# Kernel tuning notes

Measured on AMD Instinct MI355X. Metric: run time of the kernel, lower is better.

## Reference

```python
import jax, jax.numpy as jnp
from jax import lax
import numpy as np

WS = 32          # window size
NUM_AA = 21      # one-hot alphabet size (hardcoded in original forward)
L = 2048         # sequence length
WIDTH = 2048
IN_SIZE = WS * NUM_AA + WS  # 704


def setup_inputs() -> dict:
    key = jax.random.key(0)
    ks = jax.random.split(key, 8)
    x = jax.random.randint(ks[0], (L,), 0, NUM_AA, dtype=jnp.int32)
    gain = np.sqrt(2.0)  # relu gain, xavier_normal init
    def xavier(k, fan_out, fan_in):
        std = gain * np.sqrt(2.0 / (fan_in + fan_out))
        return jax.random.normal(k, (fan_out, fan_in), dtype=jnp.float32) * std
    inp = {"x": x}
    dims = [(WIDTH, IN_SIZE), (WIDTH, WIDTH), (WIDTH, WIDTH), (WIDTH, WIDTH), (WIDTH, WIDTH), (1, WIDTH)]
    for i, (fo, fi) in enumerate(dims):
        inp[f"W{i}"] = xavier(ks[i + 1], fo, fi)
        inp[f"b{i}"] = jnp.zeros((fo,), dtype=jnp.float32)
    return inp


def reference(x, W0, b0, W1, b1, W2, b2, W3, b3, W4, b4, W5, b5):
    Ws = (W0, W1, W2, W3, W4, W5)
    bs = (b0, b1, b2, b3, b4, b5)
    n = x.shape[0]
    # one-hot features; the sliding window of the last WS one-hots is
    onehot = jax.nn.one_hot(x, NUM_AA, dtype=jnp.float32)          # [n, 21]
    padded = jnp.concatenate([jnp.zeros((WS - 1, NUM_AA), jnp.float32), onehot], axis=0)
    idx = jnp.arange(n)[:, None] + jnp.arange(WS)[None, :]          # [n, WS]
    xfeat = padded[idx].reshape(n, WS * NUM_AA)                     # [n, 672]

    def step(y_window, xf):
        # y_window: last WS predictions (init zeros, matching original)
        h = jnp.concatenate([xf, y_window])                         # [704]
        for W, b in zip(Ws, bs):
            h = jax.nn.relu(W @ h + b)  # relu after EVERY layer incl. output
        y_window = jnp.concatenate([y_window[1:], h])               # h: [1]
        return y_window, h[0]

    _, ys = lax.scan(step, jnp.zeros((WS,), jnp.float32), xfeat)
    return ys  # [n] predictions, equivalent of torch.cat(y_pred[ws:])
```

## Files before the change

### kernel.cpp

```cpp
#include <hip/hip_runtime.h>
#include <stdint.h>


typedef uint32_t u32;
typedef unsigned long long ull;
typedef _Float16 half_t;
typedef _Float16 half2_t __attribute__((ext_vector_type(2)));

#define L_SEQ 2048
#define WIDTH 2048
#define WS    32
#define NAA   21
#define INS   704
#define NB    256
#define NREP  16
#define SLP_IDLE 20
#define N_IDLE   3

__device__ __forceinline__ float h2f(u32 b){
  union { unsigned short u; half_t h; } c; c.u = (unsigned short)(b & 0xffffu);
  return (float)c.h;
}
__device__ __forceinline__ u32 f2h(float f){
  union { unsigned short u; half_t h; } c; c.h = (half_t)f;
  return (u32)c.u;
}
__device__ __forceinline__ float fdot2f(u32 a, u32 b, float c){
#if __has_builtin(__builtin_amdgcn_fdot2)
  union { u32 u; half2_t v; } ca, cb; ca.u = a; cb.u = b;
  return __builtin_amdgcn_fdot2(ca.v, cb.v, c, false);
#else
  return c + h2f(a)*h2f(b) + h2f(a>>16)*h2f(b>>16);
#endif
}
__device__ __forceinline__ u32 aload(const u32* p){
  return __hip_atomic_load(const_cast<u32*>(p), __ATOMIC_RELAXED, __HIP_MEMORY_SCOPE_AGENT);
}
__device__ __forceinline__ void astore(u32* p, u32 v){
  __hip_atomic_store(p, v, __ATOMIC_RELAXED, __HIP_MEMORY_SCOPE_AGENT);
}
__device__ __forceinline__ ull aload64(const ull* p){
  return __hip_atomic_load(const_cast<ull*>(p), __ATOMIC_RELAXED, __HIP_MEMORY_SCOPE_AGENT);
}
__device__ __forceinline__ void astore64(ull* p, ull v){
  __hip_atomic_store(p, v, __ATOMIC_RELAXED, __HIP_MEMORY_SCOPE_AGENT);
}

__global__ void k_wt(const float* __restrict__ W0, float* __restrict__ W0T){
  int tid = blockIdx.x*256 + threadIdx.x;
  if (tid < INS*WIDTH){
    int c = tid >> 11, i = tid & 2047;
    W0T[(size_t)c*WIDTH + i] = W0[(size_t)i*INS + c];
  }
}

__global__ void k_wc(const float* __restrict__ A, const float* __restrict__ B,
                     const float* __restrict__ C, const float* __restrict__ D,
                     uint4* __restrict__ Wp){
  int b = blockIdx.x; int l = b >> 11; int r = b & 2047; int j = threadIdx.x;
  const float* S = (l==0)?A:(l==1)?B:(l==2)?C:D;
  const float* row = S + (size_t)r*WIDTH;
  u32 o[4];
  #pragma unroll
  for (int q=0;q<4;++q)
    o[q] = f2h(row[256*(2*q)+j]) | (f2h(row[256*(2*q+1)+j]) << 16);
  Wp[(size_t)b*256 + j] = make_uint4(o[0],o[1],o[2],o[3]);
}

__global__ void k_c0(const int* __restrict__ x, const float* __restrict__ W0T,
                     const float* __restrict__ b0, uint4* __restrict__ c0p){
  int t = blockIdx.x, j = threadIdx.x;
  __shared__ int cidx[WS];
  if (j < WS){
    int s = t - (WS-1) + j;
    cidx[j] = (s >= 0) ? (NAA*j + x[s]) : -1;
  }
  __syncthreads();
  float acc[8];
  #pragma unroll
  for (int k=0;k<8;++k) acc[k] = b0[256*k + j];
  for (int m=0;m<WS;++m){
    int c = cidx[m];
    if (c >= 0){
      const float* col = W0T + (size_t)c*WIDTH;
      #pragma unroll
      for (int k=0;k<8;++k) acc[k] += col[256*k + j];
    }
  }
  u32 o[4];
  #pragma unroll
  for (int q=0;q<4;++q) o[q] = f2h(acc[2*q]) | (f2h(acc[2*q+1]) << 16);
  c0p[(size_t)t*256 + j] = make_uint4(o[0],o[1],o[2],o[3]);
}

__global__ void k_wy(const float* __restrict__ W0, u32* __restrict__ wyb){
  int b = blockIdx.x; int k = b >> 4, p = b & 15; int j = threadIdx.x;
  int col = 256*k + j;
  float a = W0[(size_t)col*INS + (INS-WS) + 2*p];
  float c = W0[(size_t)col*INS + (INS-WS) + 2*p + 1];
  wyb[(size_t)b*256 + j] = f2h(a) | (f2h(c) << 16);
}

__global__ void k_reset(u32* __restrict__ hr, u32* __restrict__ pr){
  int tid = blockIdx.x*256 + threadIdx.x;
  if (tid < 3*NREP*2048) hr[tid] = 0xFFFFFFFFu;
  if (tid < 8192)        pr[tid] = 0xFFFFFFFFu;
}

__global__ __launch_bounds__(256, 1) void k_main(
    const float* __restrict__ W0,
    const float* __restrict__ b1, const float* __restrict__ b2,
    const float* __restrict__ b3, const float* __restrict__ b4,
    const float* __restrict__ W5, const float* __restrict__ b5p,
    const uint4* __restrict__ Wp, const uint4* __restrict__ c0p,
    const u32* __restrict__ wyb,
    u32* hrep, ull* prep, float* __restrict__ out)
{
  const int j  = threadIdx.x;
  const int X  = blockIdx.x;
  const int g  = X >> 6;
  const int Xl = X & 63;
  const int lw = j & 63;
  const int w  = j >> 6;
  const int r  = j & 31;

  __shared__ float red[2][4][32];
  __shared__ float bias_lds[32];

  uint4 wreg[32];
  #pragma unroll
  for (int i=0;i<32;++i)
    wreg[i] = Wp[((size_t)g*2048 + 32*Xl + i)*256 + j];

  const float* bp = (g==0)?b1:(g==1)?b2:(g==2)?b3:b4;
  if (j < 32) bias_lds[j] = bp[32*Xl + j];
  float w5r = 0.f;
  if (g == 3) w5r = W5[32*Xl + r];

  u32 hh[4];

  auto dotsbfly = [&](int buf){
    float c32[32];
    #pragma unroll
    for (int i=0;i<32;++i){
      float a = 0.f;
      a = fdot2f(wreg[i].x, hh[0], a);
      a = fdot2f(wreg[i].y, hh[1], a);
      a = fdot2f(wreg[i].z, hh[2], a);
      a = fdot2f(wreg[i].w, hh[3], a);
      c32[i] = a;
    }
    float c16[16];
    #pragma unroll
    for (int i=0;i<16;++i){
      float v = c32[2*i]   + __shfl_xor(c32[2*i],   1);
      float u = c32[2*i+1] + __shfl_xor(c32[2*i+1], 1);
      c16[i] = (lw & 1) ? u : v;
    }
    float c8[8];
    #pragma unroll
    for (int i=0;i<8;++i){
      float v = c16[2*i]   + __shfl_xor(c16[2*i],   2);
      float u = c16[2*i+1] + __shfl_xor(c16[2*i+1], 2);
      c8[i] = (lw & 2) ? u : v;
    }
    float c4[4];
    #pragma unroll
    for (int i=0;i<4;++i){
      float v = c8[2*i]   + __shfl_xor(c8[2*i],   4);
      float u = c8[2*i+1] + __shfl_xor(c8[2*i+1], 4);
      c4[i] = (lw & 4) ? u : v;
    }
    float c2[2];
    #pragma unroll
    for (int i=0;i<2;++i){
      float v = c4[2*i]   + __shfl_xor(c4[2*i],   8);
      float u = c4[2*i+1] + __shfl_xor(c4[2*i+1], 8);
      c2[i] = (lw & 8) ? u : v;
    }
    float v1 = c2[0] + __shfl_xor(c2[0], 16);
    float u1 = c2[1] + __shfl_xor(c2[1], 16);
    float c1 = (lw & 16) ? u1 : v1;
    float tot = c1 + __shfl_xor(c1, 32);
    if (lw < 32) red[buf][w][lw] = tot;
  };

  auto pollrec = [&](const u32* base, u32 tag, u32 (&rec)[8]){
    for(;;){
      #pragma unroll
      for (int k=0;k<8;++k) rec[k] = aload(base + 256*k);
      bool ok = true;
      #pragma unroll
      for (int k=0;k<8;++k) ok &= ((rec[k] >> 16) == tag);
      if (ok) break;
    }
  };

  for (int i=0;i<g;++i) __builtin_amdgcn_s_sleep(SLP_IDLE);

  if (g == 3){
    const u32* base = hrep + ((size_t)2*NREP + (Xl>>2))*2048 + j;
    #pragma unroll 1
    for (int t=0; t<L_SEQ; ++t){
      const int buf = t & 1;
      u32 rec[8];
      pollrec(base, (u32)t, rec);
      #pragma unroll
      for (int q=0;q<4;++q) hh[q] = (rec[2*q] & 0xffffu) | (rec[2*q+1] << 16);
      dotsbfly(buf);
      __syncthreads();
      float s = fmaxf(red[buf][0][r]+red[buf][1][r]+red[buf][2][r]+red[buf][3][r]
                      + bias_lds[r], 0.f);
      float pp = s * w5r;
      pp += __shfl_xor(pp, 1);
      pp += __shfl_xor(pp, 2);
      pp += __shfl_xor(pp, 4);
      pp += __shfl_xor(pp, 8);
      pp += __shfl_xor(pp, 16);
      if (w == 0)
        astore64(prep + (size_t)lw*64 + Xl,
                 ((ull)(u32)t << 32) | (ull)__float_as_uint(pp));
      for (int i=0;i<N_IDLE;++i) __builtin_amdgcn_s_sleep(SLP_IDLE);
    }
  } else if (g > 0){
    const u32* base = hrep + ((size_t)(g-1)*NREP + (Xl>>2))*2048 + j;
    u32* dst = hrep + (size_t)g*NREP*2048;
    #pragma unroll 1
    for (int t=0; t<L_SEQ; ++t){
      const int buf = t & 1;
      u32 rec[8];
      pollrec(base, (u32)t, rec);
      #pragma unroll
      for (int q=0;q<4;++q) hh[q] = (rec[2*q] & 0xffffu) | (rec[2*q+1] << 16);
      dotsbfly(buf);
      __syncthreads();
      float s = fmaxf(red[buf][0][r]+red[buf][1][r]+red[buf][2][r]+red[buf][3][r]
                      + bias_lds[r], 0.f);
      u32 rv = ((u32)t << 16) | f2h(s);
      astore(dst + (size_t)((j>>5)    )*2048 + 32*Xl + r, rv);
      astore(dst + (size_t)((j>>5) + 8)*2048 + 32*Xl + r, rv);
      for (int i=0;i<N_IDLE;++i) __builtin_amdgcn_s_sleep(SLP_IDLE);
    }
  } else {
    float w31v[8];
    #pragma unroll
    for (int k=0;k<8;++k)
      w31v[k] = W0[(size_t)(256*k + j)*INS + (INS-1)];
    const float b5v = b5p[0];
    u32 yqp[16];
    #pragma unroll
    for (int p=0;p<16;++p) yqp[p] = 0u;
    float u_part[8];
    #pragma unroll
    for (int k=0;k<8;++k) u_part[k] = 0.f;
    const ull* yb = prep + (size_t)Xl*64 + lw;
    u32* dst = hrep;

    #pragma unroll 1
    for (int t=0; t<L_SEQ; ++t){
      const int buf = t & 1;
      uint4 c0v = c0p[(size_t)t*256 + j];
      float y = 0.f;
      if (t > 0){
        const u32 tag = (u32)(t-1);
        ull v;
        for(;;){ v = aload64(yb); if ((u32)(v >> 32) == tag) break; }
        float p = __uint_as_float((u32)v);
        #pragma unroll
        for (int d=1; d<64; d<<=1) p += __shfl_xor(p, d);
        y = fmaxf(p + b5v, 0.f);
        if (X == 0 && j == 0) out[t-1] = y;
        yqp[15] |= (f2h(y) << 16);
      }
      {
        u32 c0h[4] = { c0v.x, c0v.y, c0v.z, c0v.w };
        float h0v[8];
        #pragma unroll
        for (int q=0;q<4;++q){
          h0v[2*q]   = fmaxf(h2f(c0h[q])       + u_part[2*q]   + w31v[2*q]*y,   0.f);
          h0v[2*q+1] = fmaxf(h2f(c0h[q] >> 16) + u_part[2*q+1] + w31v[2*q+1]*y, 0.f);
        }
        #pragma unroll
        for (int q=0;q<4;++q) hh[q] = f2h(h0v[2*q]) | (f2h(h0v[2*q+1]) << 16);
      }
      dotsbfly(buf);
      __syncthreads();
      float s = fmaxf(red[buf][0][r]+red[buf][1][r]+red[buf][2][r]+red[buf][3][r]
                      + bias_lds[r], 0.f);
      u32 rv = ((u32)t << 16) | f2h(s);
      astore(dst + (size_t)((j>>5)    )*2048 + 32*Xl + r, rv);
      astore(dst + (size_t)((j>>5) + 8)*2048 + 32*Xl + r, rv);
      {
        #pragma unroll
        for (int p=0;p<15;++p) yqp[p] = (yqp[p] >> 16) | (yqp[p+1] << 16);
        yqp[15] = (yqp[15] >> 16);
        #pragma unroll
        for (int k=0;k<8;++k){
          float a = 0.f;
          #pragma unroll
          for (int p=0;p<16;++p)
            a = fdot2f(wyb[(size_t)(16*k+p)*256 + j], yqp[p], a);
          u_part[k] = a;
        }
      }
      for (int i=0;i<N_IDLE;++i) __builtin_amdgcn_s_sleep(SLP_IDLE);
    }

    if (X == 0 && j < 64){
      const u32 tag = (u32)(L_SEQ-1);
      ull v;
      for(;;){ v = aload64(yb); if ((u32)(v >> 32) == tag) break; }
      float p = __uint_as_float((u32)v);
      #pragma unroll
      for (int d=1; d<64; d<<=1) p += __shfl_xor(p, d);
      if (j == 0) out[L_SEQ-1] = fmaxf(p + b5v, 0.f);
    }
  }
}

extern "C" void kernel_launch(void* const* d_in, const int* in_sizes, int n_in,
                              void* d_out, int out_size, void* d_ws, size_t ws_size,
                              hipStream_t stream) {
  (void)in_sizes; (void)n_in; (void)out_size; (void)ws_size;
  const int*   x  = (const int*)  d_in[0];
  const float* W0 = (const float*)d_in[1];
  const float* b0 = (const float*)d_in[2];
  const float* W1 = (const float*)d_in[3];
  const float* b1 = (const float*)d_in[4];
  const float* W2 = (const float*)d_in[5];
  const float* b2 = (const float*)d_in[6];
  const float* W3 = (const float*)d_in[7];
  const float* b3 = (const float*)d_in[8];
  const float* W4 = (const float*)d_in[9];
  const float* b4 = (const float*)d_in[10];
  const float* W5 = (const float*)d_in[11];
  const float* b5 = (const float*)d_in[12];
  float* out = (float*)d_out;
  char*  ws  = (char*)d_ws;

  constexpr size_t OFF_WP  = 0;
  constexpr size_t OFF_C0  = 33554432;
  constexpr size_t OFF_W0T = 41943040;
  constexpr size_t OFF_HR  = 41943040;
  constexpr size_t OFF_PR  = 42336256;
  constexpr size_t OFF_WY  = 47710208;

  uint4* Wp  = (uint4*)(ws + OFF_WP);
  uint4* c0p = (uint4*)(ws + OFF_C0);
  float* W0T = (float*)(ws + OFF_W0T);
  u32*   hr  = (u32*)  (ws + OFF_HR);
  u32*   pr  = (u32*)  (ws + OFF_PR);
  ull*   prq = (ull*)  (ws + OFF_PR);
  u32*   wyb = (u32*)  (ws + OFF_WY);

  k_wt   <<<5632, 256, 0, stream>>>(W0, W0T);
  k_wc   <<<8192, 256, 0, stream>>>(W1, W2, W3, W4, Wp);
  k_c0   <<<2048, 256, 0, stream>>>(x, W0T, b0, c0p);
  k_wy   <<<128,  256, 0, stream>>>(W0, wyb);
  k_reset<<<384,  256, 0, stream>>>(hr, pr);
  k_main <<<NB,   256, 0, stream>>>(W0, b1, b2, b3, b4, W5, b5,
                                    Wp, c0p, wyb, hr, prq, out);
}
```

Measured before the change: 19.66 ms.

## Replace fixed idle sleeps with adaptive pre-poll backoff and contiguous 64-bit polling

Removes the fixed per-step s_sleep idle loops and instead sleeps adaptively before polling, raising the pre-sleep when polls keep failing and lowering it when data is already ready. The activation layout is changed so each thread owns 8 contiguous hidden units, which lets the poll read four 64-bit words instead of eight strided 32-bit ones. The precompute kernels (W packing, c0, wy) are updated to the new layout with vectorized loads. The aim is less memory-spin contention across the pipelined layer blocks without idling when data is ready, at the risk of the adaptive sleep overshooting on the serial critical path.

```diff
diff --git a/kernel.cpp b/kernel.cpp
--- a/kernel.cpp
+++ b/kernel.cpp
@@ -14,8 +14,7 @@
 #define INS   704
 #define NB    256
 #define NREP  16
-#define SLP_IDLE 20
-#define N_IDLE   3
+#define PRE_CAP 36
 
 __device__ __forceinline__ float h2f(u32 b){
   union { unsigned short u; half_t h; } c; c.u = (unsigned short)(b & 0xffffu);
@@ -45,6 +44,9 @@
 __device__ __forceinline__ void astore64(ull* p, ull v){
   __hip_atomic_store(p, v, __ATOMIC_RELAXED, __HIP_MEMORY_SCOPE_AGENT);
 }
+__device__ __forceinline__ void sleepn(int v){
+  for (int i=0;i<v;++i) __builtin_amdgcn_s_sleep(8);
+}
 
 __global__ void k_wt(const float* __restrict__ W0, float* __restrict__ W0T){
   int tid = blockIdx.x*256 + threadIdx.x;
@@ -59,11 +61,13 @@
                      uint4* __restrict__ Wp){
   int b = blockIdx.x; int l = b >> 11; int r = b & 2047; int j = threadIdx.x;
   const float* S = (l==0)?A:(l==1)?B:(l==2)?C:D;
-  const float* row = S + (size_t)r*WIDTH;
+  const float2* r2 = (const float2*)(S + (size_t)r*WIDTH + 8*j);
   u32 o[4];
   #pragma unroll
-  for (int q=0;q<4;++q)
-    o[q] = f2h(row[256*(2*q)+j]) | (f2h(row[256*(2*q+1)+j]) << 16);
+  for (int q=0;q<4;++q){
+    float2 v = r2[q];
+    o[q] = f2h(v.x) | (f2h(v.y) << 16);
+  }
   Wp[(size_t)b*256 + j] = make_uint4(o[0],o[1],o[2],o[3]);
 }
 
@@ -77,14 +81,17 @@
   }
   __syncthreads();
   float acc[8];
-  #pragma unroll
-  for (int k=0;k<8;++k) acc[k] = b0[256*k + j];
+  const float4* bp = (const float4*)(b0 + 8*j);
+  float4 b00 = bp[0], b01 = bp[1];
+  acc[0]=b00.x; acc[1]=b00.y; acc[2]=b00.z; acc[3]=b00.w;
+  acc[4]=b01.x; acc[5]=b01.y; acc[6]=b01.z; acc[7]=b01.w;
   for (int m=0;m<WS;++m){
     int c = cidx[m];
     if (c >= 0){
-      const float* col = W0T + (size_t)c*WIDTH;
-      #pragma unroll
-      for (int k=0;k<8;++k) acc[k] += col[256*k + j];
+      const float4* cp = (const float4*)(W0T + (size_t)c*WIDTH + 8*j);
+      float4 u0 = cp[0], u1 = cp[1];
+      acc[0]+=u0.x; acc[1]+=u0.y; acc[2]+=u0.z; acc[3]+=u0.w;
+      acc[4]+=u1.x; acc[5]+=u1.y; acc[6]+=u1.z; acc[7]+=u1.w;
     }
   }
   u32 o[4];
@@ -94,8 +101,8 @@
 }
 
 __global__ void k_wy(const float* __restrict__ W0, u32* __restrict__ wyb){
-  int b = blockIdx.x; int k = b >> 4, p = b & 15; int j = threadIdx.x;
-  int col = 256*k + j;
+  int b = blockIdx.x; int e = b >> 4, p = b & 15; int j = threadIdx.x;
+  int col = 8*j + e;
   float a = W0[(size_t)col*INS + (INS-WS) + 2*p];
   float c = W0[(size_t)col*INS + (INS-WS) + 2*p + 1];
   wyb[(size_t)b*256 + j] = f2h(a) | (f2h(c) << 16);
@@ -138,6 +145,7 @@
   if (g == 3) w5r = W5[32*Xl + r];
 
   u32 hh[4];
+  int pre = 0;
 
   auto dotsbfly = [&](int buf){
     float c32[32];
@@ -185,28 +193,49 @@
     if (lw < 32) red[buf][w][lw] = tot;
   };
 
-  auto pollrec = [&](const u32* base, u32 tag, u32 (&rec)[8]){
+  auto pollrec = [&](const ull* b64, u32 tag) -> int {
+    int fails = -1;
+    ull r0,r1,r2,r3;
     for(;;){
-      #pragma unroll
-      for (int k=0;k<8;++k) rec[k] = aload(base + 256*k);
-      bool ok = true;
-      #pragma unroll
-      for (int k=0;k<8;++k) ok &= ((rec[k] >> 16) == tag);
+      ++fails;
+      r0 = aload64(b64+0); r1 = aload64(b64+1);
+      r2 = aload64(b64+2); r3 = aload64(b64+3);
+      u32 t01 = ((u32)r0 >> 16)       & 0xffffu;
+      bool ok = (t01 == tag)
+             & (((u32)(r0>>32) >> 16) == tag)
+             & (((u32)r1       >> 16) == tag)
+             & (((u32)(r1>>32) >> 16) == tag)
+             & (((u32)r2       >> 16) == tag)
+             & (((u32)(r2>>32) >> 16) == tag)
+             & (((u32)r3       >> 16) == tag)
+             & (((u32)(r3>>32) >> 16) == tag);
       if (ok) break;
-    }
+      __builtin_amdgcn_s_sleep(2);
+    }
+    hh[0] = ((u32)r0 & 0xffffu) | ((u32)(r0>>32) << 16);
+    hh[1] = ((u32)r1 & 0xffffu) | ((u32)(r1>>32) << 16);
+    hh[2] = ((u32)r2 & 0xffffu) | ((u32)(r2>>32) << 16);
+    hh[3] = ((u32)r3 & 0xffffu) | ((u32)(r3>>32) << 16);
+    return fails;
   };
 
-  for (int i=0;i<g;++i) __builtin_amdgcn_s_sleep(SLP_IDLE);
+  auto adapt = [&](int fails){
+    if (fails == 0){ if (pre > 0) --pre; }
+    else if (fails >= 2){
+      int add = fails - 1; if (add > 4) add = 4;
+      pre += add; if (pre > PRE_CAP) pre = PRE_CAP;
+    }
+  };
+
+  for (int i=0;i<g;++i) __builtin_amdgcn_s_sleep(16);
 
   if (g == 3){
-    const u32* base = hrep + ((size_t)2*NREP + (Xl>>2))*2048 + j;
+    const ull* b64 = (const ull*)(hrep + ((size_t)2*NREP + (Xl>>2))*2048) + 4*j;
     #pragma unroll 1
     for (int t=0; t<L_SEQ; ++t){
       const int buf = t & 1;
-      u32 rec[8];
-      pollrec(base, (u32)t, rec);
-      #pragma unroll
-      for (int q=0;q<4;++q) hh[q] = (rec[2*q] & 0xffffu) | (rec[2*q+1] << 16);
+      sleepn(pre);
+      adapt(pollrec(b64, (u32)t));
       dotsbfly(buf);
       __syncthreads();
       float s = fmaxf(red[buf][0][r]+red[buf][1][r]+red[buf][2][r]+red[buf][3][r]
@@ -220,18 +249,15 @@
       if (w == 0)
         astore64(prep + (size_t)lw*64 + Xl,
                  ((ull)(u32)t << 32) | (ull)__float_as_uint(pp));
-      for (int i=0;i<N_IDLE;++i) __builtin_amdgcn_s_sleep(SLP_IDLE);
     }
   } else if (g > 0){
-    const u32* base = hrep + ((size_t)(g-1)*NREP + (Xl>>2))*2048 + j;
+    const ull* b64 = (const ull*)(hrep + ((size_t)(g-1)*NREP + (Xl>>2))*2048) + 4*j;
     u32* dst = hrep + (size_t)g*NREP*2048;
     #pragma unroll 1
     for (int t=0; t<L_SEQ; ++t){
       const int buf = t & 1;
-      u32 rec[8];
-      pollrec(base, (u32)t, rec);
-      #pragma unroll
-      for (int q=0;q<4;++q) hh[q] = (rec[2*q] & 0xffffu) | (rec[2*q+1] << 16);
+      sleepn(pre);
+      adapt(pollrec(b64, (u32)t));
       dotsbfly(buf);
       __syncthreads();
       float s = fmaxf(red[buf][0][r]+red[buf][1][r]+red[buf][2][r]+red[buf][3][r]
@@ -239,22 +265,22 @@
       u32 rv = ((u32)t << 16) | f2h(s);
       astore(dst + (size_t)((j>>5)    )*2048 + 32*Xl + r, rv);
       astore(dst + (size_t)((j>>5) + 8)*2048 + 32*Xl + r, rv);
-      for (int i=0;i<N_IDLE;++i) __builtin_amdgcn_s_sleep(SLP_IDLE);
     }
   } else {
     float w31v[8];
     #pragma unroll
-    for (int k=0;k<8;++k)
-      w31v[k] = W0[(size_t)(256*k + j)*INS + (INS-1)];
+    for (int e=0;e<8;++e)
+      w31v[e] = W0[(size_t)(8*j + e)*INS + (INS-1)];
     const float b5v = b5p[0];
     u32 yqp[16];
     #pragma unroll
     for (int p=0;p<16;++p) yqp[p] = 0u;
     float u_part[8];
     #pragma unroll
-    for (int k=0;k<8;++k) u_part[k] = 0.f;
+    for (int e=0;e<8;++e) u_part[e] = 0.f;
     const ull* yb = prep + (size_t)Xl*64 + lw;
     u32* dst = hrep;
+    int preY = 0;
 
     #pragma unroll 1
     for (int t=0; t<L_SEQ; ++t){
@@ -263,8 +289,11 @@
       float y = 0.f;
       if (t > 0){
         const u32 tag = (u32)(t-1);
-        ull v;
-        for(;;){ v = aload64(yb); if ((u32)(v >> 32) == tag) break; }
+        sleepn(preY);
+        int fy = -1; ull v;
+        do { ++fy; v = aload64(yb); } while ((u32)(v >> 32) != tag);
+        if (fy == 0){ if (preY > 0) --preY; }
+        else if (fy >= 4){ preY += 1; if (preY > PRE_CAP) preY = PRE_CAP; }
         float p = __uint_as_float((u32)v);
         #pragma unroll
         for (int d=1; d<64; d<<=1) p += __shfl_xor(p, d);
@@ -295,15 +324,14 @@
         for (int p=0;p<15;++p) yqp[p] = (yqp[p] >> 16) | (yqp[p+1] << 16);
         yqp[15] = (yqp[15] >> 16);
         #pragma unroll
-        for (int k=0;k<8;++k){
+        for (int e=0;e<8;++e){
           float a = 0.f;
           #pragma unroll
           for (int p=0;p<16;++p)
-            a = fdot2f(wyb[(size_t)(16*k+p)*256 + j], yqp[p], a);
-          u_part[k] = a;
+            a = fdot2f(wyb[(size_t)(16*e+p)*256 + j], yqp[p], a);
+          u_part[e] = a;
         }
       }
-      for (int i=0;i<N_IDLE;++i) __builtin_amdgcn_s_sleep(SLP_IDLE);
     }
 
     if (X == 0 && j < 64){
```

After: 21.04 ms. +7.0%, slower.

## Give each wave its own rows in layers 2-4, removing cross-wave LDS reduction

Applied to the files above, without the earlier changes.

For layer groups 1-3, weights are repacked in contiguous row order so that each wave owns 8 output rows and reads the full input vector. It polls 64-bit records and reduces across the wave with shuffles, which removes the __syncthreads and LDS reduction from each timestep. The last layer now publishes four partial sums per block (one per wave), and the layer-0 blocks poll and sum those four. Each lane's polling load grows from 8 to 16 atomic 64-bit reads per step, and the workspace layout for the partials changes.

```diff
diff --git a/kernel.cpp b/kernel.cpp
--- a/kernel.cpp
+++ b/kernel.cpp
@@ -54,17 +54,28 @@
   }
 }
 
-__global__ void k_wc(const float* __restrict__ A, const float* __restrict__ B,
-                     const float* __restrict__ C, const float* __restrict__ D,
-                     uint4* __restrict__ Wp){
-  int b = blockIdx.x; int l = b >> 11; int r = b & 2047; int j = threadIdx.x;
-  const float* S = (l==0)?A:(l==1)?B:(l==2)?C:D;
-  const float* row = S + (size_t)r*WIDTH;
+__global__ void k_wc0(const float* __restrict__ W1, uint4* __restrict__ Wp){
+  int r = blockIdx.x; int j = threadIdx.x;
+  const float* row = W1 + (size_t)r*WIDTH;
   u32 o[4];
   #pragma unroll
   for (int q=0;q<4;++q)
     o[q] = f2h(row[256*(2*q)+j]) | (f2h(row[256*(2*q+1)+j]) << 16);
-  Wp[(size_t)b*256 + j] = make_uint4(o[0],o[1],o[2],o[3]);
+  Wp[(size_t)r*256 + j] = make_uint4(o[0],o[1],o[2],o[3]);
+}
+
+__global__ void k_wc2(const float* __restrict__ B, const float* __restrict__ C,
+                      const float* __restrict__ D, uint4* __restrict__ Wp){
+  int b = blockIdx.x; int l3 = b >> 11; int r = b & 2047; int j = threadIdx.x;
+  const float* S = (l3==0)?B:(l3==1)?C:D;
+  const float2* p2 = (const float2*)(S + (size_t)r*WIDTH + 8*j);
+  u32 o[4];
+  #pragma unroll
+  for (int q=0;q<4;++q){
+    float2 v = p2[q];
+    o[q] = f2h(v.x) | (f2h(v.y) << 16);
+  }
+  Wp[((size_t)(1+l3)*2048 + r)*256 + j] = make_uint4(o[0],o[1],o[2],o[3]);
 }
 
 __global__ void k_c0(const int* __restrict__ x, const float* __restrict__ W0T,
@@ -104,7 +115,7 @@
 __global__ void k_reset(u32* __restrict__ hr, u32* __restrict__ pr){
   int tid = blockIdx.x*256 + threadIdx.x;
   if (tid < 3*NREP*2048) hr[tid] = 0xFFFFFFFFu;
-  if (tid < 8192)        pr[tid] = 0xFFFFFFFFu;
+  if (tid < 64*256*2)    pr[tid] = 0xFFFFFFFFu;
 }
 
 __global__ __launch_bounds__(256, 1) void k_main(
@@ -122,126 +133,103 @@
   const int Xl = X & 63;
   const int lw = j & 63;
   const int w  = j >> 6;
-  const int r  = j & 31;
 
   __shared__ float red[2][4][32];
   __shared__ float bias_lds[32];
 
-  uint4 wreg[32];
-  #pragma unroll
-  for (int i=0;i<32;++i)
-    wreg[i] = Wp[((size_t)g*2048 + 32*Xl + i)*256 + j];
-
-  const float* bp = (g==0)?b1:(g==1)?b2:(g==2)?b3:b4;
-  if (j < 32) bias_lds[j] = bp[32*Xl + j];
-  float w5r = 0.f;
-  if (g == 3) w5r = W5[32*Xl + r];
-
-  u32 hh[4];
-
-  auto dotsbfly = [&](int buf){
-    float c32[32];
+  for (int i=0;i<g;++i) __builtin_amdgcn_s_sleep(SLP_IDLE);
+
+  if (g > 0){
+    const int rowl = 32*Xl + 8*w + (lw & 7);
+    uint4 wreg[32];
     #pragma unroll
-    for (int i=0;i<32;++i){
-      float a = 0.f;
-      a = fdot2f(wreg[i].x, hh[0], a);
-      a = fdot2f(wreg[i].y, hh[1], a);
-      a = fdot2f(wreg[i].z, hh[2], a);
-      a = fdot2f(wreg[i].w, hh[3], a);
-      c32[i] = a;
-    }
-    float c16[16];
-    #pragma unroll
-    for (int i=0;i<16;++i){
-      float v = c32[2*i]   + __shfl_xor(c32[2*i],   1);
-      float u = c32[2*i+1] + __shfl_xor(c32[2*i+1], 1);
-      c16[i] = (lw & 1) ? u : v;
-    }
-    float c8[8];
-    #pragma unroll
-    for (int i=0;i<8;++i){
-      float v = c16[2*i]   + __shfl_xor(c16[2*i],   2);
-      float u = c16[2*i+1] + __shfl_xor(c16[2*i+1], 2);
-      c8[i] = (lw & 2) ? u : v;
-    }
-    float c4[4];
-    #pragma unroll
-    for (int i=0;i<4;++i){
-      float v = c8[2*i]   + __shfl_xor(c8[2*i],   4);
-      float u = c8[2*i+1] + __shfl_xor(c8[2*i+1], 4);
-      c4[i] = (lw & 4) ? u : v;
-    }
-    float c2[2];
-    #pragma unroll
-    for (int i=0;i<2;++i){
-      float v = c4[2*i]   + __shfl_xor(c4[2*i],   8);
-      float u = c4[2*i+1] + __shfl_xor(c4[2*i+1], 8);
-      c2[i] = (lw & 8) ? u : v;
-    }
-    float v1 = c2[0] + __shfl_xor(c2[0], 16);
-    float u1 = c2[1] + __shfl_xor(c2[1], 16);
-    float c1 = (lw & 16) ? u1 : v1;
-    float tot = c1 + __shfl_xor(c1, 32);
-    if (lw < 32) red[buf][w][lw] = tot;
-  };
-
-  auto pollrec = [&](const u32* base, u32 tag, u32 (&rec)[8]){
-    for(;;){
-      #pragma unroll
-      for (int k=0;k<8;++k) rec[k] = aload(base + 256*k);
-      bool ok = true;
-      #pragma unroll
-      for (int k=0;k<8;++k) ok &= ((rec[k] >> 16) == tag);
-      if (ok) break;
-    }
-  };
-
-  for (int i=0;i<g;++i) __builtin_amdgcn_s_sleep(SLP_IDLE);
-
-  if (g == 3){
-    const u32* base = hrep + ((size_t)2*NREP + (Xl>>2))*2048 + j;
+    for (int rr=0;rr<8;++rr)
+      #pragma unroll
+      for (int q=0;q<4;++q)
+        wreg[rr*4+q] = Wp[((size_t)g*2048 + 32*Xl + 8*w + rr)*256 + 4*lw + q];
+    const float* bp = (g==1)?b2:(g==2)?b3:b4;
+    const float bv  = bp[rowl];
+    const float w5v = (g==3) ? W5[rowl] : 0.f;
+
+    const ull* b64 = (const ull*)(hrep + ((size_t)(g-1)*NREP + (Xl>>2))*2048)
+                     + 16*lw;
+    u32* dst = hrep + (size_t)g*NREP*2048;
+
+    u32 hh[16];
     #pragma unroll 1
     for (int t=0; t<L_SEQ; ++t){
-      const int buf = t & 1;
-      u32 rec[8];
-      pollrec(base, (u32)t, rec);
-      #pragma unroll
-      for (int q=0;q<4;++q) hh[q] = (rec[2*q] & 0xffffu) | (rec[2*q+1] << 16);
-      dotsbfly(buf);
-      __syncthreads();
-      float s = fmaxf(red[buf][0][r]+red[buf][1][r]+red[buf][2][r]+red[buf][3][r]
-                      + bias_lds[r], 0.f);
-      float pp = s * w5r;
-      pp += __shfl_xor(pp, 1);
-      pp += __shfl_xor(pp, 2);
-      pp += __shfl_xor(pp, 4);
-      pp += __shfl_xor(pp, 8);
-      pp += __shfl_xor(pp, 16);
-      if (w == 0)
-        astore64(prep + (size_t)lw*64 + Xl,
-                 ((ull)(u32)t << 32) | (ull)__float_as_uint(pp));
-      for (int i=0;i<N_IDLE;++i) __builtin_amdgcn_s_sleep(SLP_IDLE);
-    }
-  } else if (g > 0){
-    const u32* base = hrep + ((size_t)(g-1)*NREP + (Xl>>2))*2048 + j;
-    u32* dst = hrep + (size_t)g*NREP*2048;
-    #pragma unroll 1
-    for (int t=0; t<L_SEQ; ++t){
-      const int buf = t & 1;
-      u32 rec[8];
-      pollrec(base, (u32)t, rec);
-      #pragma unroll
-      for (int q=0;q<4;++q) hh[q] = (rec[2*q] & 0xffffu) | (rec[2*q+1] << 16);
-      dotsbfly(buf);
-      __syncthreads();
-      float s = fmaxf(red[buf][0][r]+red[buf][1][r]+red[buf][2][r]+red[buf][3][r]
-                      + bias_lds[r], 0.f);
-      u32 rv = ((u32)t << 16) | f2h(s);
-      astore(dst + (size_t)((j>>5)    )*2048 + 32*Xl + r, rv);
-      astore(dst + (size_t)((j>>5) + 8)*2048 + 32*Xl + r, rv);
+      const u32 tag = (u32)t;
+      ull r64[16];
+      for(;;){
+        #pragma unroll
+        for (int k=0;k<16;++k) r64[k] = aload64(b64 + k);
+        bool ok = true;
+        #pragma unroll
+        for (int k=0;k<16;++k)
+          ok &= (((u32)r64[k] >> 16) == tag) & (((u32)(r64[k]>>32) >> 16) == tag);
+        if (ok) break;
+      }
+      #pragma unroll
+      for (int k=0;k<16;++k)
+        hh[k] = ((u32)r64[k] & 0xffffu) | ((u32)(r64[k]>>32) << 16);
+
+      float acc[8];
+      #pragma unroll
+      for (int rr=0;rr<8;++rr){
+        float a = 0.f;
+        #pragma unroll
+        for (int q=0;q<4;++q){
+          uint4 W = wreg[rr*4+q];
+          a = fdot2f(W.x, hh[4*q+0], a);
+          a = fdot2f(W.y, hh[4*q+1], a);
+          a = fdot2f(W.z, hh[4*q+2], a);
+          a = fdot2f(W.w, hh[4*q+3], a);
+        }
+        acc[rr] = a;
+      }
+      float m[4];
+      #pragma unroll
+      for (int i=0;i<4;++i){
+        float ta = acc[2*i]   + __shfl_xor(acc[2*i],   1);
+        float tb = acc[2*i+1] + __shfl_xor(acc[2*i+1], 1);
+        m[i] = (lw & 1) ? tb : ta;
+      }
+      float n[2];
+      #pragma unroll
+      for (int i=0;i<2;++i){
+        float ta = m[2*i]   + __shfl_xor(m[2*i],   2);
+        float tb = m[2*i+1] + __shfl_xor(m[2*i+1], 2);
+        n[i] = (lw & 2) ? tb : ta;
+      }
+      float ta = n[0] + __shfl_xor(n[0], 4);
+      float tb = n[1] + __shfl_xor(n[1], 4);
+      float tot = (lw & 4) ? tb : ta;
+      tot += __shfl_xor(tot, 8);
+      tot += __shfl_xor(tot, 16);
+      tot += __shfl_xor(tot, 32);
+
+      float s = fmaxf(tot + bv, 0.f);
+      if (g < 3){
+        u32 rv = (tag << 16) | f2h(s);
+        astore(dst + (size_t)(lw>>3)*2048 + rowl, rv);
+        astore(dst + (size_t)((lw>>3)+8)*2048 + rowl, rv);
+      } else {
+        float pp = s * w5v;
+        pp += __shfl_xor(pp, 1);
+        pp += __shfl_xor(pp, 2);
+        pp += __shfl_xor(pp, 4);
+        astore64(prep + (size_t)lw*256 + 4*Xl + w,
+                 ((ull)tag << 32) | (ull)__float_as_uint(pp));
+      }
       for (int i=0;i<N_IDLE;++i) __builtin_amdgcn_s_sleep(SLP_IDLE);
     }
   } else {
+    const int r = j & 31;
+    uint4 wreg[32];
+    #pragma unroll
+    for (int i=0;i<32;++i)
+      wreg[i] = Wp[((size_t)32*Xl + i)*256 + j];
+    if (j < 32) bias_lds[j] = b1[32*Xl + j];
     float w31v[8];
     #pragma unroll
     for (int k=0;k<8;++k)
@@ -253,8 +241,55 @@
     float u_part[8];
     #pragma unroll
     for (int k=0;k<8;++k) u_part[k] = 0.f;
-    const ull* yb = prep + (size_t)Xl*64 + lw;
+    const ull* yb = prep + (size_t)Xl*256 + 4*lw;
     u32* dst = hrep;
+    u32 hh[4];
+
+    auto dotsbfly = [&](int buf){
+      float c32[32];
+      #pragma unroll
+      for (int i=0;i<32;++i){
+        float a = 0.f;
+        a = fdot2f(wreg[i].x, hh[0], a);
+        a = fdot2f(wreg[i].y, hh[1], a);
+        a = fdot2f(wreg[i].z, hh[2], a);
+        a = fdot2f(wreg[i].w, hh[3], a);
+        c32[i] = a;
+      }
+      float c16[16];
+      #pragma unroll
+      for (int i=0;i<16;++i){
+        float v = c32[2*i]   + __shfl_xor(c32[2*i],   1);
+        float u = c32[2*i+1] + __shfl_xor(c32[2*i+1], 1);
+        c16[i] = (lw & 1) ? u : v;
+      }
+      float c8[8];
+      #pragma unroll
+      for (int i=0;i<8;++i){
+        float v = c16[2*i]   + __shfl_xor(c16[2*i],   2);
+        float u = c16[2*i+1] + __shfl_xor(c16[2*i+1], 2);
+        c8[i] = (lw & 2) ? u : v;
+      }
+      float c4[4];
+      #pragma unroll
+      for (int i=0;i<4;++i){
+        float v = c8[2*i]   + __shfl_xor(c8[2*i],   4);
+        float u = c8[2*i+1] + __shfl_xor(c8[2*i+1], 4);
+        c4[i] = (lw & 4) ? u : v;
+      }
+      float c2[2];
+      #pragma unroll
+      for (int i=0;i<2;++i){
+        float v = c4[2*i]   + __shfl_xor(c4[2*i],   8);
+        float u = c4[2*i+1] + __shfl_xor(c4[2*i+1], 8);
+        c2[i] = (lw & 8) ? u : v;
+      }
+      float v1 = c2[0] + __shfl_xor(c2[0], 16);
+      float u1 = c2[1] + __shfl_xor(c2[1], 16);
+      float c1 = (lw & 16) ? u1 : v1;
+      float tot = c1 + __shfl_xor(c1, 32);
+      if (lw < 32) red[buf][w][lw] = tot;
+    };
 
     #pragma unroll 1
     for (int t=0; t<L_SEQ; ++t){
@@ -263,9 +298,15 @@
       float y = 0.f;
       if (t > 0){
         const u32 tag = (u32)(t-1);
-        ull v;
-        for(;;){ v = aload64(yb); if ((u32)(v >> 32) == tag) break; }
-        float p = __uint_as_float((u32)v);
+        ull v0,v1,v2,v3;
+        for(;;){
+          v0 = aload64(yb+0); v1 = aload64(yb+1);
+          v2 = aload64(yb+2); v3 = aload64(yb+3);
+          if (((u32)(v0>>32)==tag) & ((u32)(v1>>32)==tag) &
+              ((u32)(v2>>32)==tag) & ((u32)(v3>>32)==tag)) break;
+        }
+        float p = __uint_as_float((u32)v0) + __uint_as_float((u32)v1)
+                + __uint_as_float((u32)v2) + __uint_as_float((u32)v3);
         #pragma unroll
         for (int d=1; d<64; d<<=1) p += __shfl_xor(p, d);
         y = fmaxf(p + b5v, 0.f);
@@ -306,11 +347,17 @@
       for (int i=0;i<N_IDLE;++i) __builtin_amdgcn_s_sleep(SLP_IDLE);
     }
 
-    if (X == 0 && j < 64){
+    if (X == 0){
       const u32 tag = (u32)(L_SEQ-1);
-      ull v;
-      for(;;){ v = aload64(yb); if ((u32)(v >> 32) == tag) break; }
-      float p = __uint_as_float((u32)v);
+      ull v0,v1,v2,v3;
+      for(;;){
+        v0 = aload64(yb+0); v1 = aload64(yb+1);
+        v2 = aload64(yb+2); v3 = aload64(yb+3);
+        if (((u32)(v0>>32)==tag) & ((u32)(v1>>32)==tag) &
+            ((u32)(v2>>32)==tag) & ((u32)(v3>>32)==tag)) break;
+      }
+      float p = __uint_as_float((u32)v0) + __uint_as_float((u32)v1)
+              + __uint_as_float((u32)v2) + __uint_as_float((u32)v3);
       #pragma unroll
       for (int d=1; d<64; d<<=1) p += __shfl_xor(p, d);
       if (j == 0) out[L_SEQ-1] = fmaxf(p + b5v, 0.f);
@@ -354,10 +401,11 @@
   u32*   wyb = (u32*)  (ws + OFF_WY);
 
   k_wt   <<<5632, 256, 0, stream>>>(W0, W0T);
-  k_wc   <<<8192, 256, 0, stream>>>(W1, W2, W3, W4, Wp);
+  k_wc0  <<<2048, 256, 0, stream>>>(W1, Wp);
+  k_wc2  <<<6144, 256, 0, stream>>>(W2, W3, W4, Wp);
   k_c0   <<<2048, 256, 0, stream>>>(x, W0T, b0, c0p);
   k_wy   <<<128,  256, 0, stream>>>(W0, wyb);
-  k_reset<<<384,  256, 0, stream>>>(hr, pr);
+  k_reset<<<512,  256, 0, stream>>>(hr, pr);
   k_main <<<NB,   256, 0, stream>>>(W0, b1, b2, b3, b4, W5, b5,
                                     Wp, c0p, wyb, hr, prq, out);
 }
```

Result: slower. 51.58 ms (+162.4%).
